# Performance work log

Hardware: AMD Instinct MI355X
Metric: run time of the kernel (lower is better)

The kernel has to match this reference:

```python
import jax, jax.numpy as jnp
import numpy as np

B, S, D, M, H, HD, V = 256, 128, 512, 150, 8, 64, 10000
LN_EPS = 1e-5

def layer_norm(x, g, b):
    mu = jnp.mean(x, axis=-1, keepdims=True)
    var = jnp.mean((x - mu) ** 2, axis=-1, keepdims=True)
    return (x - mu) * jax.lax.rsqrt(var + LN_EPS) * g + b

def setup_inputs() -> dict:
    key = jax.random.key(0)
    ks = jax.random.split(key, 20)
    s = 0.02
    return {
        'x': jax.random.randint(ks[0], (B, S), 0, V),
        'emb': jax.random.normal(ks[1], (V, D)) * s,
        'W1': jax.random.normal(ks[2], (M, D, D)) * s,   # [mode, out, in]
        'b1': jnp.zeros((M, D)),
        'ln1_g': jnp.ones((M, D)),
        'ln1_b': jnp.zeros((M, D)),
        'W2': jax.random.normal(ks[3], (M, D, D)) * s,
        'b2': jnp.zeros((M, D)),
        'dbias': jax.random.normal(ks[4], (M, D)) * 0.01,
        'in_proj_w': jax.random.normal(ks[5], (3 * D, D)) * s,
        'in_proj_b': jnp.zeros((3 * D,)),
        'out_proj_w': jax.random.normal(ks[6], (D, D)) * s,
        'out_proj_b': jnp.zeros((D,)),
        'norm_g': jnp.ones((D,)),
        'norm_b': jnp.zeros((D,)),
        'dec_w1': jax.random.normal(ks[7], (D // 2, D)) * s,
        'dec_b1': jnp.zeros((D // 2,)),
        'dec_w2': jax.random.normal(ks[8], (V, D // 2)) * s,
        'dec_b2': jnp.zeros((V,)),
    }

def reference(x, emb, W1, b1, ln1_g, ln1_b, W2, b2, dbias,
              in_proj_w, in_proj_b, out_proj_w, out_proj_b,
              norm_g, norm_b, dec_w1, dec_b1, dec_w2, dec_b2):
    # shared embedding: [B,S] -> [B,D]
    e = jnp.take(emb, x, axis=0).mean(axis=1)
    # 150 mode heads as grouped GEMMs: Linear -> LN -> ReLU -> Linear + bias
    h = jnp.einsum('bd,mod->bmo', e, W1) + b1                    # [B,M,D]
    h = layer_norm(h, ln1_g, ln1_b)
    h = jax.nn.relu(h)                                            # dropout = identity (eval)
    mode_out = jnp.einsum('bmd,mod->bmo', h, W2) + b2 + dbias     # [B,M,D]
    # cross-mode self-attention (torch MultiheadAttention, batch_first)
    qkv = mode_out @ in_proj_w.T + in_proj_b                      # [B,M,3D]
    q, k, v = jnp.split(qkv, 3, axis=-1)
    q = q.reshape(B, M, H, HD); k = k.reshape(B, M, H, HD); v = v.reshape(B, M, H, HD)
    scores = jnp.einsum('bqhd,bkhd->bhqk', q, k) / np.sqrt(HD)
    attn = jax.nn.softmax(scores, axis=-1)
    o = jnp.einsum('bhqk,bkhd->bqhd', attn, v).reshape(B, M, D)
    attended = o @ out_proj_w.T + out_proj_b                      # [B,M,D]
    # gating mask: active_modes=None -> all ones, so gated == attended
    agg = layer_norm(attended.sum(axis=1), norm_g, norm_b)        # [B,D]
    # decoder: Linear -> ReLU -> Linear
    dec = jax.nn.relu(agg @ dec_w1.T + dec_b1)
    return dec @ dec_w2.T + dec_b2                                # [B,V]
```

## Files before the change

### kernel.cpp

```cpp
#include <hip/hip_runtime.h>

typedef __attribute__((ext_vector_type(8))) short s16x8;
typedef __attribute__((ext_vector_type(8))) unsigned short u16x8;
typedef __attribute__((ext_vector_type(4))) float f32x4;

#define LN_EPS 1e-5f

__device__ inline float bf2f(unsigned short u) {
    union { unsigned int i; float f; } x; x.i = ((unsigned int)u) << 16; return x.f;
}
__device__ inline unsigned short f2bf(float f) {
    unsigned int u = __builtin_bit_cast(unsigned int, f);
    u += 0x7FFFu + ((u >> 16) & 1u);
    return (unsigned short)(u >> 16);
}
__device__ inline unsigned int cvt_pk_bf16(float lo, float hi) {
    unsigned int r;
    asm("v_cvt_pk_bf16_f32 %0, %1, %2" : "=v"(r) : "v"(lo), "v"(hi));
    return r;
}
typedef __attribute__((address_space(1))) const unsigned int as1_u32;
typedef __attribute__((address_space(3))) unsigned int as3_u32;
__device__ inline void gl2lds16(const void* g, void* l) {
    __builtin_amdgcn_global_load_lds((as1_u32*)g, (as3_u32*)l, 16, 0, 0);
}

__device__ inline void cvt_stream(const float* __restrict__ src,
                                  unsigned short* __restrict__ dst,
                                  int n8, int lb, int nb, int tid)
{
    int i = lb * 256 + tid;
    const int stride = nb * 256;
    for (; i < n8; i += stride) {
        const float4 a = ((const float4*)src)[2 * i];
        const float4 b = ((const float4*)src)[2 * i + 1];
        union { unsigned int u[4]; u16x8 v; } r;
        r.u[0] = cvt_pk_bf16(a.x, a.y);
        r.u[1] = cvt_pk_bf16(a.z, a.w);
        r.u[2] = cvt_pk_bf16(b.x, b.y);
        r.u[3] = cvt_pk_bf16(b.z, b.w);
        ((u16x8*)dst)[i] = r.v;
    }
}

__global__ __launch_bounds__(256) void prep_kernel(
    const int* __restrict__ x, const float* __restrict__ emb,
    unsigned short* __restrict__ e,
    const float* __restrict__ w1, unsigned short* __restrict__ w1b,
    const float* __restrict__ ipw, unsigned short* __restrict__ ipwb,
    const float* __restrict__ opw, unsigned short* __restrict__ opwb,
    const float* __restrict__ dw1, unsigned short* __restrict__ dw1b,
    const float* __restrict__ dw2, unsigned short* __restrict__ dw2b)
{
    const int tid = threadIdx.x;
    int b = blockIdx.x;
    if (b < 256) {
        __shared__ int xs[128];
        if (tid < 128) xs[tid] = x[b * 128 + tid];
        __syncthreads();
        float s0 = 0.f, s1 = 0.f;
        for (int i = 0; i < 128; ++i) {
            const float* r = emb + (size_t)xs[i] * 512;
            s0 += r[tid]; s1 += r[tid + 256];
        }
        e[(size_t)b * 512 + tid] = f2bf(s0 * (1.f / 128.f));
        e[(size_t)b * 512 + tid + 256] = f2bf(s1 * (1.f / 128.f));
        return;
    }
    b -= 256;
    if (b < 2048) { cvt_stream(w1, w1b, 150 * 512 * 512 / 8, b, 2048, tid); return; }
    b -= 2048;
    if (b < 384) { cvt_stream(ipw, ipwb, 1536 * 512 / 8, b, 384, tid); return; }
    b -= 384;
    if (b < 128) { cvt_stream(opw, opwb, 512 * 512 / 8, b, 128, tid); return; }
    b -= 128;
    if (b < 64) { cvt_stream(dw1, dw1b, 256 * 512 / 8, b, 64, tid); return; }
    b -= 64;
    cvt_stream(dw2, dw2b, 10000 * 256 / 8, b, 1280, tid);
}
#define PREP_BLOCKS (256 + 2048 + 384 + 128 + 64 + 1280)

template<int K, bool RELU, bool F32OUT>
__global__ __launch_bounds__(256, 4) void gemm_bf_kernel(
    const unsigned short* __restrict__ A,
    const unsigned short* __restrict__ Wb,
    const float* __restrict__ bias1,
    const float* __restrict__ bias2,
    float bias_scale,
    void* __restrict__ Cv,
    int N, int gx, int gy, int ngemm,
    size_t strideA_mode, size_t lda,
    size_t strideW_mode, size_t strideB_mode,
    size_t strideC_mode, size_t ldc,
    const float* __restrict__ cvt_src, unsigned short* __restrict__ cvt_dst,
    int cvt_n8)
{
    constexpr int NSTEP = K / 32;
    const int tid = threadIdx.x;
    const int wgid = blockIdx.x;

    if (wgid >= ngemm) {
        cvt_stream(cvt_src, cvt_dst, cvt_n8, wgid - ngemm, gridDim.x - ngemm, tid);
        return;
    }

    const int q8 = ngemm >> 3, r8 = ngemm & 7;
    const int xcd = wgid & 7, sub = wgid >> 3;
    int p = (xcd < r8 ? xcd * (q8 + 1) : r8 * (q8 + 1) + (xcd - r8) * q8) + sub;
    const int bx = p % gx; p /= gx;
    const int by = p % gy;
    const int bz = p / gy;
    const int n0 = bx * 128, r0 = by * 128;

    __shared__ __align__(16) unsigned char lds[2][16384];

    const int lane = tid & 63, wid = tid >> 6;
    const int fr = lane & 15, ks = lane >> 4;
    const int wr = (wid >> 1) * 64, wc = (wid & 1) * 64;

    const int Ia0 = (wid * 2 + 0) * 64 + lane;
    const int Ia1 = (wid * 2 + 1) * 64 + lane;
    const int ar0 = Ia0 >> 2, ac0 = (Ia0 & 3) ^ (ar0 & 3);
    const int ar1 = Ia1 >> 2, ac1 = (Ia1 & 3) ^ (ar1 & 3);
    const unsigned char* Aslab = (const unsigned char*)(A + (size_t)bz * strideA_mode);
    const unsigned char* aSrc0 = Aslab + (size_t)(r0 + ar0) * lda * 2 + ac0 * 16;
    const unsigned char* aSrc1 = Aslab + (size_t)(r0 + ar1) * lda * 2 + ac1 * 16;
    const unsigned char* Wslab = (const unsigned char*)(Wb + (size_t)bz * strideW_mode);
    const int br0 = min(n0 + ar0, N - 1), br1 = min(n0 + ar1, N - 1);
    const unsigned char* bSrc0 = Wslab + (size_t)br0 * K * 2 + ac0 * 16;
    const unsigned char* bSrc1 = Wslab + (size_t)br1 * K * 2 + ac1 * 16;

    f32x4 acc[4][4];
#pragma unroll
    for (int i = 0; i < 4; ++i)
#pragma unroll
        for (int j = 0; j < 4; ++j)
#pragma unroll
            for (int r = 0; r < 4; ++r) acc[i][j][r] = 0.f;

    auto stage = [&](int buf, int t) {
        gl2lds16(aSrc0 + (size_t)t * 64, &lds[buf][(wid * 2 + 0) * 1024]);
        gl2lds16(aSrc1 + (size_t)t * 64, &lds[buf][(wid * 2 + 1) * 1024]);
        gl2lds16(bSrc0 + (size_t)t * 64, &lds[buf][8192 + (wid * 2 + 0) * 1024]);
        gl2lds16(bSrc1 + (size_t)t * 64, &lds[buf][8192 + (wid * 2 + 1) * 1024]);
    };

    auto compute = [&](int buf) {
        const unsigned char* Ab = &lds[buf][0];
        const unsigned char* Bb = &lds[buf][8192];
        const int co = (ks ^ (fr & 3)) << 4;
        s16x8 af[4], bfr[4];
#pragma unroll
        for (int mi = 0; mi < 4; ++mi)
            af[mi] = *(const s16x8*)(Ab + (wr + mi * 16 + fr) * 64 + co);
#pragma unroll
        for (int ni = 0; ni < 4; ++ni)
            bfr[ni] = *(const s16x8*)(Bb + (wc + ni * 16 + fr) * 64 + co);
#pragma unroll
        for (int mi = 0; mi < 4; ++mi)
#pragma unroll
            for (int ni = 0; ni < 4; ++ni)
                acc[mi][ni] = __builtin_amdgcn_mfma_f32_16x16x32_bf16(af[mi], bfr[ni], acc[mi][ni], 0, 0, 0);
    };

    stage(0, 0);
    __syncthreads();

    for (int t = 0; t < NSTEP; t += 2) {
        stage(1, t + 1);
        compute(0);
        __syncthreads();
        if (t + 2 < NSTEP) stage(0, t + 2);
        compute(1);
        __syncthreads();
    }

    if (!F32OUT) {
        unsigned short* Cl = (unsigned short*)&lds[0][0];
#pragma unroll
        for (int ni = 0; ni < 4; ++ni) {
            const int col = n0 + wc + ni * 16 + fr;
            float bsum = 0.f;
            if (bias1) bsum += bias_scale * bias1[(size_t)bz * strideB_mode + col];
            if (bias2) bsum += bias2[(size_t)bz * strideB_mode + col];
#pragma unroll
            for (int mi = 0; mi < 4; ++mi)
#pragma unroll
                for (int r = 0; r < 4; ++r) {
                    float v = acc[mi][ni][r] + bsum;
                    if (RELU) v = fmaxf(v, 0.f);
                    Cl[(wr + mi * 16 + ks * 4 + r) * 128 + wc + ni * 16 + fr] = f2bf(v);
                }
        }
        __syncthreads();
        unsigned short* Cg = (unsigned short*)Cv + (size_t)bz * strideC_mode;
#pragma unroll
        for (int it = 0; it < 8; ++it) {
            const int c = it * 256 + tid;
            const int row = c >> 4, ch = c & 15;
            u16x8 v = *(const u16x8*)(&Cl[row * 128 + ch * 8]);
            *(u16x8*)(Cg + (size_t)(r0 + row) * ldc + n0 + ch * 8) = v;
        }
    } else {
#pragma unroll
        for (int ni = 0; ni < 4; ++ni) {
            const int col = n0 + wc + ni * 16 + fr;
            if (col < N) {
                float bsum = 0.f;
                if (bias1) bsum += bias_scale * bias1[(size_t)bz * strideB_mode + col];
                if (bias2) bsum += bias2[(size_t)bz * strideB_mode + col];
#pragma unroll
                for (int mi = 0; mi < 4; ++mi)
#pragma unroll
                    for (int r = 0; r < 4; ++r) {
                        const int row = r0 + wr + mi * 16 + ks * 4 + r;
                        float v = acc[mi][ni][r] + bsum;
                        if (RELU) v = fmaxf(v, 0.f);
                        ((float*)Cv)[(size_t)bz * strideC_mode + (size_t)row * ldc + col] = v;
                    }
            }
        }
    }
}

template<bool RELU>
__global__ __launch_bounds__(256) void ln_kernel(
    const unsigned short* __restrict__ X,
    const float* __restrict__ G,
    const float* __restrict__ Bt,
    unsigned short* __restrict__ Y,
    int M)
{
    const int row = blockIdx.x;
    const int m = row % M;
    const unsigned short* xr = X + (size_t)row * 512;
    unsigned short* yr = Y + (size_t)row * 512;
    const int tid = threadIdx.x;
    const float x0 = bf2f(xr[tid]), x1 = bf2f(xr[tid + 256]);
    float s = x0 + x1, q = x0 * x0 + x1 * x1;
#pragma unroll
    for (int off = 32; off; off >>= 1) {
        s += __shfl_xor(s, off);
        q += __shfl_xor(q, off);
    }
    __shared__ float red[4][2];
    const int wid = tid >> 6, lane = tid & 63;
    if (lane == 0) { red[wid][0] = s; red[wid][1] = q; }
    __syncthreads();
    s = red[0][0] + red[1][0] + red[2][0] + red[3][0];
    q = red[0][1] + red[1][1] + red[2][1] + red[3][1];
    const float mu = s * (1.f / 512.f);
    const float var = q * (1.f / 512.f) - mu * mu;
    const float rstd = rsqrtf(var + LN_EPS);
    const float* g = G + (size_t)m * 512;
    const float* bt = Bt + (size_t)m * 512;
    float y0 = (x0 - mu) * rstd * g[tid] + bt[tid];
    float y1 = (x1 - mu) * rstd * g[tid + 256] + bt[tid + 256];
    if (RELU) { y0 = fmaxf(y0, 0.f); y1 = fmaxf(y1, 0.f); }
    yr[tid] = f2bf(y0);
    yr[tid + 256] = f2bf(y1);
}

#define KP 72
#define VP 168
__global__ __launch_bounds__(256) void attn_mfma_kernel(
    const unsigned short* __restrict__ qkv, unsigned short* __restrict__ o_att)
{
    const int b = blockIdx.x >> 3, h = blockIdx.x & 7;
    __shared__ __align__(16) unsigned short k_s[160 * KP];
    __shared__ __align__(16) unsigned short v_t[64 * VP];
    __shared__ __align__(16) unsigned short p_s[4][16 * VP];
    const int tid = threadIdx.x, lane = tid & 63, wid = tid >> 6;
    const int fr = lane & 15, ks = lane >> 4;
    const size_t base = (size_t)b * (150 * 1536) + h * 64;

    for (int idx = tid; idx < 160 * 8; idx += 256) {
        const int r = idx >> 3, c8 = (idx & 7) * 8;
        u16x8 v;
        if (r < 150) v = *(const u16x8*)(qkv + base + (size_t)r * 1536 + 512 + c8);
        else {
#pragma unroll
            for (int j = 0; j < 8; ++j) v[j] = 0;
        }
        *(u16x8*)(&k_s[r * KP + c8]) = v;
    }
    for (int idx = tid; idx < 160 * 8; idx += 256) {
        const int c8 = idx / 160, r = idx - c8 * 160;
        u16x8 v;
        if (r < 150) v = *(const u16x8*)(qkv + base + (size_t)r * 1536 + 1024 + c8 * 8);
        else {
#pragma unroll
            for (int j = 0; j < 8; ++j) v[j] = 0;
        }
#pragma unroll
        for (int j = 0; j < 8; ++j) v_t[(c8 * 8 + j) * VP + r] = v[j];
    }
    __syncthreads();

    unsigned short* pw = &p_s[wid][0];

    for (int qt = wid; qt < 10; qt += 4) {
        const int qr = (qt * 16 + fr < 150) ? qt * 16 + fr : 149;
        const unsigned short* qp = qkv + base + (size_t)qr * 1536;
        s16x8 qa0 = *(const s16x8*)(qp + ks * 8);
        s16x8 qa1 = *(const s16x8*)(qp + 32 + ks * 8);

        f32x4 acc[10];
#pragma unroll
        for (int t = 0; t < 10; ++t)
#pragma unroll
            for (int r = 0; r < 4; ++r) acc[t][r] = 0.f;
#pragma unroll
        for (int t = 0; t < 10; ++t) {
            s16x8 kb0 = *(const s16x8*)(&k_s[(t * 16 + fr) * KP + ks * 8]);
            s16x8 kb1 = *(const s16x8*)(&k_s[(t * 16 + fr) * KP + 32 + ks * 8]);
            acc[t] = __builtin_amdgcn_mfma_f32_16x16x32_bf16(qa0, kb0, acc[t], 0, 0, 0);
            acc[t] = __builtin_amdgcn_mfma_f32_16x16x32_bf16(qa1, kb1, acc[t], 0, 0, 0);
        }

        const bool v9 = (fr < 6);
        float inv[4];
#pragma unroll
        for (int i = 0; i < 4; ++i) {
            float m = -1e30f;
#pragma unroll
            for (int t = 0; t < 9; ++t) m = fmaxf(m, acc[t][i]);
            if (v9) m = fmaxf(m, acc[9][i]);
#pragma unroll
            for (int off = 1; off < 16; off <<= 1) m = fmaxf(m, __shfl_xor(m, off));
            float s = 0.f;
#pragma unroll
            for (int t = 0; t < 10; ++t) {
                float e = 0.f;
                if (t < 9 || v9) e = __expf(0.125f * (acc[t][i] - m));
                s += e;
                pw[(ks * 4 + i) * VP + t * 16 + fr] = f2bf(e);
            }
#pragma unroll
            for (int off = 1; off < 16; off <<= 1) s += __shfl_xor(s, off);
            inv[i] = 1.f / s;
        }

        f32x4 o[4];
#pragma unroll
        for (int dt = 0; dt < 4; ++dt)
#pragma unroll
            for (int r = 0; r < 4; ++r) o[dt][r] = 0.f;
#pragma unroll
        for (int kc = 0; kc < 5; ++kc) {
            s16x8 pa = *(const s16x8*)(&pw[fr * VP + kc * 32 + ks * 8]);
#pragma unroll
            for (int dt = 0; dt < 4; ++dt) {
                s16x8 vb = *(const s16x8*)(&v_t[(dt * 16 + fr) * VP + kc * 32 + ks * 8]);
                o[dt] = __builtin_amdgcn_mfma_f32_16x16x32_bf16(pa, vb, o[dt], 0, 0, 0);
            }
        }

#pragma unroll
        for (int dt = 0; dt < 4; ++dt) {
            const int d = h * 64 + dt * 16 + fr;
#pragma unroll
            for (int i = 0; i < 4; ++i) {
                const int q = qt * 16 + ks * 4 + i;
                if (q < 150)
                    o_att[((size_t)(b * 150 + q)) * 512 + d] = f2bf(o[dt][i] * inv[i]);
            }
        }
    }
}

__global__ __launch_bounds__(512) void osum_kernel(
    const unsigned short* __restrict__ o_att, unsigned short* __restrict__ osum)
{
    const int b = blockIdx.x, tid = threadIdx.x;
    float s = 0.f;
    const unsigned short* p = o_att + (size_t)b * 150 * 512 + tid;
    for (int mm = 0; mm < 150; ++mm) s += bf2f(p[(size_t)mm * 512]);
    osum[(size_t)b * 512 + tid] = f2bf(s);
}

extern "C" void kernel_launch(void* const* d_in, const int* in_sizes, int n_in,
                              void* d_out, int out_size, void* d_ws, size_t ws_size,
                              hipStream_t stream)
{
    (void)in_sizes; (void)n_in; (void)out_size; (void)ws_size;

    const int*   x          = (const int*)d_in[0];
    const float* emb        = (const float*)d_in[1];
    const float* W1         = (const float*)d_in[2];
    const float* b1         = (const float*)d_in[3];
    const float* ln1_g      = (const float*)d_in[4];
    const float* ln1_b      = (const float*)d_in[5];
    const float* W2         = (const float*)d_in[6];
    const float* b2         = (const float*)d_in[7];
    const float* dbias      = (const float*)d_in[8];
    const float* in_proj_w  = (const float*)d_in[9];
    const float* in_proj_b  = (const float*)d_in[10];
    const float* out_proj_w = (const float*)d_in[11];
    const float* out_proj_b = (const float*)d_in[12];
    const float* norm_g     = (const float*)d_in[13];
    const float* norm_b     = (const float*)d_in[14];
    const float* dec_w1     = (const float*)d_in[15];
    const float* dec_b1     = (const float*)d_in[16];
    const float* dec_w2     = (const float*)d_in[17];
    const float* dec_b2     = (const float*)d_in[18];

    char* ws = (char*)d_ws;
    unsigned short* e_bf  = (unsigned short*)(ws + 0x0);
    unsigned short* osum  = (unsigned short*)(ws + 0x40000);
    unsigned short* att1  = (unsigned short*)(ws + 0x80000);
    unsigned short* agg   = (unsigned short*)(ws + 0xC0000);
    unsigned short* dec1  = (unsigned short*)(ws + 0x100000);
    unsigned short* h1    = (unsigned short*)(ws + 0x200000);
    unsigned short* mo    = (unsigned short*)(ws + 0x2800000);
    unsigned short* qkvf  = (unsigned short*)(ws + 0x4E00000);
    unsigned short* Wbf1  = (unsigned short*)(ws + 0xBE80000);
    unsigned short* Wbf2  = (unsigned short*)(ws + 0x10980000);
    unsigned short* ipwbf = (unsigned short*)(ws + 0x15480000);
    unsigned short* opwbf = (unsigned short*)(ws + 0x15600000);
    unsigned short* dw1bf = (unsigned short*)(ws + 0x15700000);
    unsigned short* dw2bf = (unsigned short*)(ws + 0x15800000);
    unsigned short* o_att = h1;

    prep_kernel<<<PREP_BLOCKS, 256, 0, stream>>>(
        x, emb, e_bf, W1, Wbf1, in_proj_w, ipwbf, out_proj_w, opwbf,
        dec_w1, dw1bf, dec_w2, dw2bf);

    gemm_bf_kernel<512, false, false><<<1200 + 2048, 256, 0, stream>>>(
        e_bf, Wbf1, b1, nullptr, 1.f, h1,
        512, 4, 2, 1200,
        (size_t)0, 512, (size_t)512 * 512, 512, 512, 76800,
        W2, Wbf2, 150 * 512 * 512 / 8);

    ln_kernel<true><<<38400, 256, 0, stream>>>(h1, ln1_g, ln1_b, h1, 150);

    gemm_bf_kernel<512, false, false><<<1200, 256, 0, stream>>>(
        h1, Wbf2, b2, dbias, 1.f, mo,
        512, 4, 2, 1200,
        (size_t)512, 76800, (size_t)512 * 512, 512, 512, 76800,
        nullptr, nullptr, 0);

    gemm_bf_kernel<512, false, false><<<3600, 256, 0, stream>>>(
        mo, ipwbf, in_proj_b, nullptr, 1.f, qkvf,
        1536, 12, 300, 3600,
        (size_t)0, 512, (size_t)0, 0, 0, 1536,
        nullptr, nullptr, 0);

    attn_mfma_kernel<<<2048, 256, 0, stream>>>(qkvf, o_att);

    osum_kernel<<<256, 512, 0, stream>>>(o_att, osum);

    gemm_bf_kernel<512, false, false><<<8, 256, 0, stream>>>(
        osum, opwbf, out_proj_b, nullptr, 150.f, att1,
        512, 4, 2, 8,
        (size_t)0, 512, (size_t)0, 0, 0, 512,
        nullptr, nullptr, 0);

    ln_kernel<false><<<256, 256, 0, stream>>>(att1, norm_g, norm_b, agg, 1);

    gemm_bf_kernel<512, true, false><<<4, 256, 0, stream>>>(
        agg, dw1bf, dec_b1, nullptr, 1.f, dec1,
        256, 2, 2, 4,
        (size_t)0, 512, (size_t)0, 0, 0, 256,
        nullptr, nullptr, 0);

    gemm_bf_kernel<256, false, true><<<158, 256, 0, stream>>>(
        dec1, dw2bf, dec_b2, nullptr, 1.f, d_out,
        10000, 79, 2, 158,
        (size_t)0, 256, (size_t)0, 0, 0, 10000,
        nullptr, nullptr, 0);
}
```

Baseline: 397.7 us.

## Fuse mode-sum reduction into attention kernel and unroll prep loads

After: 398.1 us. No clear change (+0.1%).

```diff
diff --git a/kernel.cpp b/kernel.cpp
--- a/kernel.cpp
+++ b/kernel.cpp
@@ -25,21 +25,33 @@
     __builtin_amdgcn_global_load_lds((as1_u32*)g, (as3_u32*)l, 16, 0, 0);
 }
 
+__device__ inline u16x8 cvt8(float4 a, float4 b) {
+    union { unsigned int u[4]; u16x8 v; } r;
+    r.u[0] = cvt_pk_bf16(a.x, a.y);
+    r.u[1] = cvt_pk_bf16(a.z, a.w);
+    r.u[2] = cvt_pk_bf16(b.x, b.y);
+    r.u[3] = cvt_pk_bf16(b.z, b.w);
+    return r.v;
+}
+
 __device__ inline void cvt_stream(const float* __restrict__ src,
                                   unsigned short* __restrict__ dst,
                                   int n8, int lb, int nb, int tid)
 {
     int i = lb * 256 + tid;
     const int stride = nb * 256;
-    for (; i < n8; i += stride) {
+    for (; i + stride < n8; i += 2 * stride) {
+        const float4 a0 = ((const float4*)src)[2 * i];
+        const float4 b0 = ((const float4*)src)[2 * i + 1];
+        const float4 a1 = ((const float4*)src)[2 * (i + stride)];
+        const float4 b1 = ((const float4*)src)[2 * (i + stride) + 1];
+        ((u16x8*)dst)[i] = cvt8(a0, b0);
+        ((u16x8*)dst)[i + stride] = cvt8(a1, b1);
+    }
+    if (i < n8) {
         const float4 a = ((const float4*)src)[2 * i];
         const float4 b = ((const float4*)src)[2 * i + 1];
-        union { unsigned int u[4]; u16x8 v; } r;
-        r.u[0] = cvt_pk_bf16(a.x, a.y);
-        r.u[1] = cvt_pk_bf16(a.z, a.w);
-        r.u[2] = cvt_pk_bf16(b.x, b.y);
-        r.u[3] = cvt_pk_bf16(b.z, b.w);
-        ((u16x8*)dst)[i] = r.v;
+        ((u16x8*)dst)[i] = cvt8(a, b);
     }
 }
 
@@ -59,9 +71,18 @@
         if (tid < 128) xs[tid] = x[b * 128 + tid];
         __syncthreads();
         float s0 = 0.f, s1 = 0.f;
-        for (int i = 0; i < 128; ++i) {
-            const float* r = emb + (size_t)xs[i] * 512;
-            s0 += r[tid]; s1 += r[tid + 256];
+#pragma unroll 1
+        for (int i = 0; i < 128; i += 4) {
+            const float* r0 = emb + (size_t)xs[i] * 512;
+            const float* r1 = emb + (size_t)xs[i + 1] * 512;
+            const float* r2 = emb + (size_t)xs[i + 2] * 512;
+            const float* r3 = emb + (size_t)xs[i + 3] * 512;
+            const float a0 = r0[tid], c0 = r0[tid + 256];
+            const float a1 = r1[tid], c1 = r1[tid + 256];
+            const float a2 = r2[tid], c2 = r2[tid + 256];
+            const float a3 = r3[tid], c3 = r3[tid + 256];
+            s0 += (a0 + a1) + (a2 + a3);
+            s1 += (c0 + c1) + (c2 + c3);
         }
         e[(size_t)b * 512 + tid] = f2bf(s0 * (1.f / 128.f));
         e[(size_t)b * 512 + tid + 256] = f2bf(s1 * (1.f / 128.f));
@@ -264,12 +285,13 @@
 #define KP 72
 #define VP 168
 __global__ __launch_bounds__(256) void attn_mfma_kernel(
-    const unsigned short* __restrict__ qkv, unsigned short* __restrict__ o_att)
+    const unsigned short* __restrict__ qkv, unsigned short* __restrict__ osum)
 {
     const int b = blockIdx.x >> 3, h = blockIdx.x & 7;
     __shared__ __align__(16) unsigned short k_s[160 * KP];
     __shared__ __align__(16) unsigned short v_t[64 * VP];
     __shared__ __align__(16) unsigned short p_s[4][16 * VP];
+    __shared__ float redsum[4][64];
     const int tid = threadIdx.x, lane = tid & 63, wid = tid >> 6;
     const int fr = lane & 15, ks = lane >> 4;
     const size_t base = (size_t)b * (150 * 1536) + h * 64;
@@ -298,6 +320,7 @@
     __syncthreads();
 
     unsigned short* pw = &p_s[wid][0];
+    float psum[4] = {0.f, 0.f, 0.f, 0.f};
 
     for (int qt = wid; qt < 10; qt += 4) {
         const int qr = (qt * 16 + fr < 150) ? qt * 16 + fr : 149;
@@ -357,26 +380,26 @@
         }
 
 #pragma unroll
-        for (int dt = 0; dt < 4; ++dt) {
-            const int d = h * 64 + dt * 16 + fr;
+        for (int dt = 0; dt < 4; ++dt)
 #pragma unroll
             for (int i = 0; i < 4; ++i) {
                 const int q = qt * 16 + ks * 4 + i;
-                if (q < 150)
-                    o_att[((size_t)(b * 150 + q)) * 512 + d] = f2bf(o[dt][i] * inv[i]);
+                if (q < 150) psum[dt] += o[dt][i] * inv[i];
             }
-        }
-    }
-}
-
-__global__ __launch_bounds__(512) void osum_kernel(
-    const unsigned short* __restrict__ o_att, unsigned short* __restrict__ osum)
-{
-    const int b = blockIdx.x, tid = threadIdx.x;
-    float s = 0.f;
-    const unsigned short* p = o_att + (size_t)b * 150 * 512 + tid;
-    for (int mm = 0; mm < 150; ++mm) s += bf2f(p[(size_t)mm * 512]);
-    osum[(size_t)b * 512 + tid] = f2bf(s);
+    }
+
+#pragma unroll
+    for (int dt = 0; dt < 4; ++dt) {
+        float v = psum[dt];
+        v += __shfl_xor(v, 16);
+        v += __shfl_xor(v, 32);
+        if (ks == 0) redsum[wid][dt * 16 + fr] = v;
+    }
+    __syncthreads();
+    if (tid < 64) {
+        const float s = redsum[0][tid] + redsum[1][tid] + redsum[2][tid] + redsum[3][tid];
+        osum[(size_t)b * 512 + h * 64 + tid] = f2bf(s);
+    }
 }
 
 extern "C" void kernel_launch(void* const* d_in, const int* in_sizes, int n_in,
@@ -420,7 +443,6 @@
     unsigned short* opwbf = (unsigned short*)(ws + 0x15600000);
     unsigned short* dw1bf = (unsigned short*)(ws + 0x15700000);
     unsigned short* dw2bf = (unsigned short*)(ws + 0x15800000);
-    unsigned short* o_att = h1;
 
     prep_kernel<<<PREP_BLOCKS, 256, 0, stream>>>(
         x, emb, e_bf, W1, Wbf1, in_proj_w, ipwbf, out_proj_w, opwbf,
@@ -446,9 +468,7 @@
         (size_t)0, 512, (size_t)0, 0, 0, 1536,
         nullptr, nullptr, 0);
 
-    attn_mfma_kernel<<<2048, 256, 0, stream>>>(qkvf, o_att);
-
-    osum_kernel<<<256, 512, 0, stream>>>(o_att, osum);
+    attn_mfma_kernel<<<2048, 256, 0, stream>>>(qkvf, osum);
 
     gemm_bf_kernel<512, false, false><<<8, 256, 0, stream>>>(
         osum, opwbf, out_proj_b, nullptr, 150.f, att1,
```
